# Kernel tuning notes

Measured on AMD Instinct MI355X. Metric: run time of the kernel, lower is better.

The kernel has to match this reference:

```python
import jax, jax.numpy as jnp
from jax import lax
import numpy as np

IMG_H = IMG_W = 1024
STRIDE = 16
FH = FW = 64
C = 512
NA = 9
IOU_T = 0.7
NEG = -1e30
NUM_CLASSES = 21
FV = 4096
POOL = 7


def _make_anchor_map():
    scales = np.array([128.0, 256.0, 512.0])
    ratios = np.array([0.5, 1.0, 2.0])
    ah = (scales[:, None] * np.sqrt(ratios)[None, :]).reshape(-1)  # (9,)
    aw = (scales[:, None] / np.sqrt(ratios)[None, :]).reshape(-1)
    cy = (np.arange(FH) + 0.5) * STRIDE
    cx = (np.arange(FW) + 0.5) * STRIDE
    amap = np.zeros((FH, FW, NA, 4), np.float32)
    amap[..., 0] = cy[:, None, None]
    amap[..., 1] = cx[None, :, None]
    amap[..., 2] = ah
    amap[..., 3] = aw
    return amap.reshape(FH, FW, NA * 4)


def setup_inputs() -> dict:
    key = jax.random.key(0)
    ks = jax.random.split(key, 10)
    flat = POOL * POOL * C
    return {
        "feature_map": jax.random.normal(ks[0], (1, C, FH, FW), jnp.float32),
        "anchor_map": jnp.asarray(_make_anchor_map()),
        "anchor_valid_map": jnp.ones((FH, FW, NA), jnp.float32),
        "rpn_conv1_w": 0.01 * jax.random.normal(ks[1], (C, C, 3, 3), jnp.float32),
        "rpn_conv1_b": jnp.zeros((C,), jnp.float32),
        "rpn_cls_w": 0.01 * jax.random.normal(ks[2], (NA, C, 1, 1), jnp.float32),
        "rpn_cls_b": jnp.zeros((NA,), jnp.float32),
        "rpn_box_w": 0.01 * jax.random.normal(ks[3], (NA * 4, C, 1, 1), jnp.float32),
        "rpn_box_b": jnp.zeros((NA * 4,), jnp.float32),
        "fc1_w": 0.01 * jax.random.normal(ks[4], (FV, flat), jnp.float32),
        "fc1_b": jnp.zeros((FV,), jnp.float32),
        "fc2_w": 0.01 * jax.random.normal(ks[5], (FV, FV), jnp.float32),
        "fc2_b": jnp.zeros((FV,), jnp.float32),
        "cls_w": 0.01 * jax.random.normal(ks[6], (NUM_CLASSES, FV), jnp.float32),
        "cls_b": jnp.zeros((NUM_CLASSES,), jnp.float32),
        "reg_w": 0.001 * jax.random.normal(ks[7], (4 * (NUM_CLASSES - 1), FV), jnp.float32),
        "reg_b": jnp.zeros((4 * (NUM_CLASSES - 1),), jnp.float32),
        "max_proposals_pre_nms": 6000,
        "max_proposals_post_nms": 300,
    }


def _conv(x, w, b):
    y = lax.conv_general_dilated(x, w, (1, 1), 'SAME',
                                 dimension_numbers=('NCHW', 'OIHW', 'NCHW'))
    return y + b[None, :, None, None]


def _roi_pool(fm, rois):
    # fm: (C,H,W); rois: (N,4) as (x1,y1,x2,y2) in pixel coords (torchvision RoIPool semantics)
    Hh, Ww = fm.shape[1], fm.shape[2]
    s = 1.0 / STRIDE
    p = jnp.arange(POOL, dtype=fm.dtype)
    hi = jnp.arange(Hh, dtype=fm.dtype)
    wi = jnp.arange(Ww, dtype=fm.dtype)

    def one(roi):
        x1 = jnp.round(roi[0] * s); y1 = jnp.round(roi[1] * s)
        x2 = jnp.round(roi[2] * s); y2 = jnp.round(roi[3] * s)
        rw = jnp.maximum(x2 - x1 + 1.0, 1.0)
        rh = jnp.maximum(y2 - y1 + 1.0, 1.0)
        bh = rh / POOL; bw = rw / POOL
        hstart = jnp.clip(jnp.floor(p * bh) + y1, 0, Hh)
        hend = jnp.clip(jnp.ceil((p + 1) * bh) + y1, 0, Hh)
        wstart = jnp.clip(jnp.floor(p * bw) + x1, 0, Ww)
        wend = jnp.clip(jnp.ceil((p + 1) * bw) + x1, 0, Ww)
        mh = (hi[None, :] >= hstart[:, None]) & (hi[None, :] < hend[:, None])  # (7,H)
        mw = (wi[None, :] >= wstart[:, None]) & (wi[None, :] < wend[:, None])  # (7,W)
        # max over w per (c,h,pw), then max over h per (c,ph,pw)
        t1 = jnp.max(jnp.where(mw[None, None, :, :], fm[:, :, None, :], NEG), axis=-1)  # (C,H,7)
        t2 = jnp.max(jnp.where(mh[None, :, :, None], t1[:, None, :, :], NEG), axis=2)   # (C,7,7)
        return jnp.where(t2 < NEG / 2, 0.0, t2)  # empty bins -> 0

    return lax.map(one, rois)  # (N,C,7,7)


def reference(feature_map, anchor_map, anchor_valid_map,
              rpn_conv1_w, rpn_conv1_b, rpn_cls_w, rpn_cls_b, rpn_box_w, rpn_box_b,
              fc1_w, fc1_b, fc2_w, fc2_b, cls_w, cls_b, reg_w, reg_b,
              max_proposals_pre_nms, max_proposals_post_nms):
    # ---- RPN heads ----
    y = jax.nn.relu(_conv(feature_map, rpn_conv1_w, rpn_conv1_b))
    scores_map = jax.nn.sigmoid(_conv(y, rpn_cls_w, rpn_cls_b)).transpose(0, 2, 3, 1)   # (1,H,W,9)
    deltas_map = _conv(y, rpn_box_w, rpn_box_b).transpose(0, 2, 3, 1)                   # (1,H,W,36)

    # ---- proposals from anchors + deltas (allow_edge_proposals=True: keep all) ----
    anchors = anchor_map.reshape(-1, 4)        # (cy,cx,h,w)
    scores = scores_map.reshape(-1)
    deltas = deltas_map.reshape(-1, 4)         # (ty,tx,th,tw)
    ctr = anchors[:, 0:2] + deltas[:, 0:2] * anchors[:, 2:4]
    sz = anchors[:, 2:4] * jnp.exp(deltas[:, 2:4])
    boxes = jnp.concatenate([ctr - 0.5 * sz, ctr + 0.5 * sz], axis=1)  # (y1,x1,y2,x2)
    hi_clip = jnp.array([IMG_H - 1, IMG_W - 1, IMG_H - 1, IMG_W - 1], boxes.dtype)
    boxes = jnp.clip(boxes, 0.0, hi_clip)

    # ---- top-k pre-NMS ----
    sc_pre, idx = lax.top_k(scores, max_proposals_pre_nms)
    bx = boxes[idx]

    # ---- NMS (IoU 0.7), score-sorted sequential suppression ----
    area = (bx[:, 2] - bx[:, 0]) * (bx[:, 3] - bx[:, 1])
    yy1 = jnp.maximum(bx[:, None, 0], bx[None, :, 0])
    xx1 = jnp.maximum(bx[:, None, 1], bx[None, :, 1])
    yy2 = jnp.minimum(bx[:, None, 2], bx[None, :, 2])
    xx2 = jnp.minimum(bx[:, None, 3], bx[None, :, 3])
    inter = jnp.clip(yy2 - yy1, 0.0) * jnp.clip(xx2 - xx1, 0.0)
    iou = inter / (area[:, None] + area[None, :] - inter + 1e-8)
    n = max_proposals_pre_nms
    jidx = jnp.arange(n)

    def body(i, sup):
        return sup | ((~sup[i]) & (iou[i] > IOU_T) & (jidx > i))

    sup = lax.fori_loop(0, n, body, jnp.zeros((n,), bool))
    kept_scores = jnp.where(sup, -jnp.inf, sc_pre)
    _, idx2 = lax.top_k(kept_scores, max_proposals_post_nms)
    proposals = lax.stop_gradient(bx[idx2])  # (N,4) (y1,x1,y2,x2); detached as in original

    # ---- detector head: RoIPool + FC stack ----
    rois = proposals[:, jnp.array([1, 0, 3, 2])]       # -> (x1,y1,x2,y2)
    pooled = _roi_pool(feature_map[0], rois)           # (N,C,7,7)
    flat = pooled.reshape(pooled.shape[0], -1)
    h1 = jax.nn.relu(flat @ fc1_w.T + fc1_b)
    h2 = jax.nn.relu(h1 @ fc2_w.T + fc2_b)
    classes = jax.nn.softmax(h2 @ cls_w.T + cls_b, axis=1)          # (N,21)
    box_deltas = h2 @ reg_w.T + reg_b                               # (N,80)
    return (scores_map, deltas_map, proposals, classes, box_deltas)
```

## Files before the change

kernel.cpp:

```cpp
#include <hip/hip_runtime.h>
#include <stdint.h>

typedef float f32x4 __attribute__((ext_vector_type(4)));
typedef short s16x8 __attribute__((ext_vector_type(8)));
typedef unsigned long long u64;

__device__ __forceinline__ unsigned short f2bf(float f) {
  union { float f; unsigned u; } v; v.f = f;
  unsigned u = v.u;
  return (unsigned short)((u + 0x7FFFu + ((u >> 16) & 1u)) >> 16);
}
__device__ __forceinline__ float bf2f(unsigned short b) {
  union { unsigned u; float f; } v; v.u = ((unsigned)b) << 16; return v.f;
}

#define CONV_ICC 8
__global__ __launch_bounds__(256, 2) void k_conv3(const float* __restrict__ fm,
                                                  const float* __restrict__ w,
                                                  float* __restrict__ ypart) {
  __shared__ float Xs[CONV_ICC * 342];
  __shared__ float Ws[CONV_ICC * 9 * 64];
  int bid = blockIdx.x;
  int s = bid & 3, ocg = (bid >> 2) & 7, sp = bid >> 5;
  int h0 = (sp >> 2) * 16, w0 = (sp & 3) * 16;
  int oc0 = ocg * 64;
  int t = threadIdx.x;
  int g = t >> 5, p = t & 31;
  int row = p >> 1, colb = (p & 1) * 8;
  float acc[8][8] = {};
  int cbase = s * 128;
  for (int chunk = 0; chunk < 16; chunk++) {
    int c0 = cbase + chunk * CONV_ICC;
    for (int idx = t; idx < CONV_ICC * 324; idx += 256) {
      int ic = idx / 324, rem = idx - ic * 324;
      int r = rem / 18, cc = rem - r * 18;
      int gy = h0 + r - 1, gx = w0 + cc - 1;
      float v = 0.f;
      if ((unsigned)gy < 64u && (unsigned)gx < 64u) v = fm[(c0 + ic) * 4096 + gy * 64 + gx];
      Xs[ic * 342 + r * 19 + cc] = v;
    }
    for (int idx = t; idx < CONV_ICC * 9 * 64; idx += 256) {
      int oc = idx & 63, rest = idx >> 6;
      int ic = rest / 9, k = rest - ic * 9;
      Ws[idx] = w[(u64)(oc0 + oc) * 4608 + (c0 + ic) * 9 + k];
    }
    __syncthreads();
    for (int ic = 0; ic < CONV_ICC; ic++) {
      const float* xb = &Xs[ic * 342 + colb];
      float xr[3][10];
      #pragma unroll
      for (int r = 0; r < 3; r++)
        #pragma unroll
        for (int j = 0; j < 10; j++)
          xr[r][j] = xb[(row + r) * 19 + j];
      #pragma unroll
      for (int kh = 0; kh < 3; kh++) {
        #pragma unroll
        for (int kw = 0; kw < 3; kw++) {
          const float* wp = &Ws[(ic * 9 + kh * 3 + kw) * 64 + g * 8];
          f32x4 wa = *(const f32x4*)wp;
          f32x4 wb = *(const f32x4*)(wp + 4);
          float wv[8] = {wa.x, wa.y, wa.z, wa.w, wb.x, wb.y, wb.z, wb.w};
          #pragma unroll
          for (int o = 0; o < 8; o++) {
            #pragma unroll
            for (int j = 0; j < 8; j++) {
              acc[o][j] += wv[o] * xr[kh][kw + j];
            }
          }
        }
      }
    }
    __syncthreads();
  }
  float* yp = ypart + (u64)s * 2097152;
  #pragma unroll
  for (int j = 0; j < 8; j++) {
    int pxg = (h0 + row) * 64 + (w0 + colb + j);
    f32x4 v0, v1;
    v0.x = acc[0][j]; v0.y = acc[1][j]; v0.z = acc[2][j]; v0.w = acc[3][j];
    v1.x = acc[4][j]; v1.y = acc[5][j]; v1.z = acc[6][j]; v1.w = acc[7][j];
    f32x4* dst = (f32x4*)&yp[(u64)pxg * 512 + oc0 + g * 8];
    dst[0] = v0; dst[1] = v1;
  }
}

__global__ __launch_bounds__(256) void k_rpn1x1(const float* __restrict__ ypart,
                                                const float* __restrict__ conv_b,
                                                const float* __restrict__ cw, const float* __restrict__ cb,
                                                const float* __restrict__ bw, const float* __restrict__ bb,
                                                float* __restrict__ out_s, float* __restrict__ out_d) {
  __shared__ float Ys[16 * 516];
  int px0 = blockIdx.x * 16;
  int t = threadIdx.x;
  for (int c = t; c < 16 * 128; c += 256) {
    int p = c >> 7, seg = c & 127;
    u64 off = (u64)(px0 + p) * 512 + seg * 4;
    f32x4 v0 = *(const f32x4*)&ypart[off];
    f32x4 v1 = *(const f32x4*)&ypart[2097152 + off];
    f32x4 v2 = *(const f32x4*)&ypart[2 * 2097152 + off];
    f32x4 v3 = *(const f32x4*)&ypart[3 * (u64)2097152 + off];
    f32x4 b = *(const f32x4*)&conv_b[seg * 4];
    f32x4 r;
    r.x = fmaxf(v0.x + v1.x + v2.x + v3.x + b.x, 0.f);
    r.y = fmaxf(v0.y + v1.y + v2.y + v3.y + b.y, 0.f);
    r.z = fmaxf(v0.z + v1.z + v2.z + v3.z + b.z, 0.f);
    r.w = fmaxf(v0.w + v1.w + v2.w + v3.w + b.w, 0.f);
    *(f32x4*)&Ys[p * 516 + seg * 4] = r;
  }
  __syncthreads();
  int px = t & 15, og = t >> 4;
  const float* yr = &Ys[px * 516];
  for (int n = og; n < 45; n += 16) {
    const float* wr = (n < 9) ? &cw[n * 512] : &bw[(n - 9) * 512];
    float acc = 0.f;
    for (int k = 0; k < 512; k += 4) {
      f32x4 wv = *(const f32x4*)&wr[k];
      acc += wv.x * yr[k] + wv.y * yr[k + 1] + wv.z * yr[k + 2] + wv.w * yr[k + 3];
    }
    int gpx = px0 + px;
    if (n < 9) {
      float s = acc + cb[n];
      out_s[gpx * 9 + n] = 1.f / (1.f + expf(-s));
    } else {
      out_d[gpx * 36 + (n - 9)] = acc + bb[n - 9];
    }
  }
}

__global__ void k_decode(const float* __restrict__ sc, const float* __restrict__ dl,
                         const float* __restrict__ amap,
                         float* __restrict__ boxes, u64* __restrict__ keys) {
  int i = blockIdx.x * 256 + threadIdx.x;
  if (i >= 65536) return;
  if (i < 36864) {
    int px = i / 9, a = i - px * 9;
    const float* A = &amap[i * 4];
    const float* D = &dl[px * 36 + a * 4];
    float cy = A[0] + D[0] * A[2];
    float cx = A[1] + D[1] * A[3];
    float hh = A[2] * expf(D[2]);
    float ww = A[3] * expf(D[3]);
    float y1 = fminf(fmaxf(cy - 0.5f * hh, 0.f), 1023.f);
    float x1 = fminf(fmaxf(cx - 0.5f * ww, 0.f), 1023.f);
    float y2 = fminf(fmaxf(cy + 0.5f * hh, 0.f), 1023.f);
    float x2 = fminf(fmaxf(cx + 0.5f * ww, 0.f), 1023.f);
    f32x4 v; v.x = y1; v.y = x1; v.z = y2; v.w = x2;
    *(f32x4*)&boxes[i * 4] = v;
    unsigned bits = __float_as_uint(sc[i]);
    u64 key = ((u64)bits << 16) | (u64)(0xFFFFu - (unsigned)i);
    keys[i] = ~key;
  } else {
    keys[i] = ~0ull;
  }
}

__global__ __launch_bounds__(1024) void k_sort_local(u64* __restrict__ keys) {
  __shared__ u64 S[8192];
  int base = blockIdx.x * 8192;
  for (int i = threadIdx.x; i < 8192; i += 1024) S[i] = keys[base + i];
  __syncthreads();
  for (int k = 2; k <= 8192; k <<= 1) {
    for (int j = k >> 1; j > 0; j >>= 1) {
      for (int p = threadIdx.x; p < 4096; p += 1024) {
        int i = ((p & ~(j - 1)) << 1) | (p & (j - 1));
        int ix = i | j;
        bool up = (((base + i) & k) == 0);
        u64 a = S[i], c = S[ix];
        if ((a > c) == up) { S[i] = c; S[ix] = a; }
      }
      __syncthreads();
    }
  }
  for (int i = threadIdx.x; i < 8192; i += 1024) keys[base + i] = S[i];
}

__global__ void k_sort_global(u64* __restrict__ keys, int k, int j) {
  int p = blockIdx.x * 256 + threadIdx.x;
  int i = ((p & ~(j - 1)) << 1) | (p & (j - 1));
  int ix = i | j;
  bool up = ((i & k) == 0);
  u64 a = keys[i], c = keys[ix];
  if ((a > c) == up) { keys[i] = c; keys[ix] = a; }
}

__global__ __launch_bounds__(1024) void k_sort_merge(u64* __restrict__ keys, int k) {
  __shared__ u64 S[8192];
  int base = blockIdx.x * 8192;
  for (int i = threadIdx.x; i < 8192; i += 1024) S[i] = keys[base + i];
  __syncthreads();
  for (int j = 4096; j > 0; j >>= 1) {
    for (int p = threadIdx.x; p < 4096; p += 1024) {
      int i = ((p & ~(j - 1)) << 1) | (p & (j - 1));
      int ix = i | j;
      bool up = (((base + i) & k) == 0);
      u64 a = S[i], c = S[ix];
      if ((a > c) == up) { S[i] = c; S[ix] = a; }
    }
    __syncthreads();
  }
  for (int i = threadIdx.x; i < 8192; i += 1024) keys[base + i] = S[i];
}

__global__ void k_gather_sorted(const u64* __restrict__ keys, const float* __restrict__ boxes,
                                float* __restrict__ bx) {
  int p = blockIdx.x * 256 + threadIdx.x;
  if (p >= 6000) return;
  u64 key = ~keys[p];
  int idx = 0xFFFF - (int)(key & 0xFFFFull);
  *(f32x4*)&bx[p * 4] = *(const f32x4*)&boxes[idx * 4];
}

__global__ __launch_bounds__(128) void k_nms_mask(const float* __restrict__ bx, u64* __restrict__ mask) {
  int i = blockIdx.x;
  int w = threadIdx.x;
  if (w >= 94) return;
  f32x4 bi = *(const f32x4*)&bx[i * 4];
  float ai = (bi.z - bi.x) * (bi.w - bi.y);
  u64 m = 0;
  int j0 = w * 64;
  for (int b = 0; b < 64; b++) {
    int j = j0 + b;
    if (j >= 6000) break;
    if (j <= i) continue;
    f32x4 bj = *(const f32x4*)&bx[j * 4];
    float yy1 = fmaxf(bi.x, bj.x), xx1 = fmaxf(bi.y, bj.y);
    float yy2 = fminf(bi.z, bj.z), xx2 = fminf(bi.w, bj.w);
    float inter = fmaxf(yy2 - yy1, 0.f) * fmaxf(xx2 - xx1, 0.f);
    float aj = (bj.z - bj.x) * (bj.w - bj.y);
    float iou = inter / (ai + aj - inter + 1e-8f);
    if (iou > 0.7f) m |= (1ull << b);
  }
  mask[i * 94 + w] = m;
}

__global__ __launch_bounds__(64) void k_nms_scan(const u64* __restrict__ mask, int* __restrict__ sel) {
  int lane = threadIdx.x;
  u64 rem0 = 0, rem1 = 0;
  int nkeep = 0;
  u64 cur0[16], cur1[16], nxt0[16], nxt1[16];
  bool l30 = (lane < 30);
  #pragma unroll
  for (int r = 0; r < 16; r++) {
    cur0[r] = mask[r * 94 + lane];
    cur1[r] = l30 ? mask[r * 94 + 64 + lane] : 0ull;
  }
  for (int c0 = 0; c0 < 6000; c0 += 16) {
    int n0 = c0 + 16;
    if (n0 < 6000) {
      #pragma unroll
      for (int r = 0; r < 16; r++) {
        nxt0[r] = mask[(n0 + r) * 94 + lane];
        nxt1[r] = l30 ? mask[(n0 + r) * 94 + 64 + lane] : 0ull;
      }
    }
    #pragma unroll
    for (int r = 0; r < 16; r++) {
      int i = c0 + r;
      int wi = i >> 6, bi = i & 63;
      u64 wv = (wi < 64) ? __shfl(rem0, wi, 64) : __shfl(rem1, wi - 64, 64);
      if (!((wv >> bi) & 1ull)) {
        if (lane == 0 && nkeep < 300) sel[nkeep] = i;
        nkeep++;
        rem0 |= cur0[r]; rem1 |= cur1[r];
      }
    }
    if (nkeep >= 300) return;
    #pragma unroll
    for (int r = 0; r < 16; r++) { cur0[r] = nxt0[r]; cur1[r] = nxt1[r]; }
  }
  __shared__ u64 remS[94];
  remS[lane] = rem0;
  if (l30) remS[64 + lane] = rem1;
  __syncthreads();
  if (lane == 0) {
    int k = nkeep;
    for (int i = 0; i < 6000 && k < 300; i++) {
      if ((remS[i >> 6] >> (i & 63)) & 1ull) sel[k++] = i;
    }
  }
}

__global__ void k_gather_prop(const int* __restrict__ sel, const float* __restrict__ bx,
                              float* __restrict__ out_p, float* __restrict__ rois) {
  int r = blockIdx.x * 64 + threadIdx.x;
  if (r >= 300) return;
  int p = sel[r];
  float y1 = bx[p * 4 + 0], x1 = bx[p * 4 + 1], y2 = bx[p * 4 + 2], x2 = bx[p * 4 + 3];
  out_p[r * 4 + 0] = y1; out_p[r * 4 + 1] = x1; out_p[r * 4 + 2] = y2; out_p[r * 4 + 3] = x2;
  rois[r * 4 + 0] = x1; rois[r * 4 + 1] = y1; rois[r * 4 + 2] = x2; rois[r * 4 + 3] = y2;
}

__global__ __launch_bounds__(256) void k_roipool(const float* __restrict__ fm,
                                                 const float* __restrict__ rois,
                                                 unsigned short* __restrict__ pooled) {
  int roi = blockIdx.x / 98;
  int seg = blockIdx.x - roi * 98;
  __shared__ int hs[7], he[7], wls[7], wle[7];
  if (threadIdx.x < 28) {
    int kind = threadIdx.x / 7, p = threadIdx.x - kind * 7;
    float x1 = rintf(rois[roi * 4 + 0] * 0.0625f);
    float y1 = rintf(rois[roi * 4 + 1] * 0.0625f);
    float x2 = rintf(rois[roi * 4 + 2] * 0.0625f);
    float y2 = rintf(rois[roi * 4 + 3] * 0.0625f);
    float rw = fmaxf(x2 - x1 + 1.f, 1.f), rh = fmaxf(y2 - y1 + 1.f, 1.f);
    float bh = rh / 7.f, bw = rw / 7.f;
    float fp = (float)p;
    if (kind == 0) hs[p]  = (int)fminf(fmaxf(floorf(fp * bh) + y1, 0.f), 64.f);
    if (kind == 1) he[p]  = (int)fminf(fmaxf(ceilf((fp + 1.f) * bh) + y1, 0.f), 64.f);
    if (kind == 2) wls[p] = (int)fminf(fmaxf(floorf(fp * bw) + x1, 0.f), 64.f);
    if (kind == 3) wle[p] = (int)fminf(fmaxf(ceilf((fp + 1.f) * bw) + x1, 0.f), 64.f);
  }
  __syncthreads();
  int o = seg * 256 + threadIdx.x;
  int c = o / 49; int cell = o - c * 49;
  int ph = cell / 7, pw = cell - ph * 7;
  int y0 = hs[ph], y1e = he[ph], x0 = wls[pw], x1e = wle[pw];
  bool any = (y1e > y0) && (x1e > x0);
  float m = -1e30f;
  const float* base = &fm[c * 4096];
  for (int yy = y0; yy < y1e; yy++)
    for (int xx = x0; xx < x1e; xx++)
      m = fmaxf(m, base[yy * 64 + xx]);
  pooled[(u64)roi * 25088 + o] = f2bf(any ? m : 0.f);
}

__global__ __launch_bounds__(512, 2) void k_gemm3(const unsigned short* __restrict__ A,
                                                  const float* __restrict__ B,
                                                  float* __restrict__ Cpre,
                                                  int K, int Kslice, int N) {
  __shared__ uint4 Ab[2][2560];
  __shared__ uint4 Bb[2][1024];
  int n0 = blockIdx.x * 128;
  int s = blockIdx.y;
  int t = threadIdx.x;
  int wave = t >> 6, lane = t & 63;
  int mg = wave & 1, ng = wave >> 1;
  int m0 = mg * 160;
  int lr = lane & 15, lk = lane >> 4;

  int am[5], aks[5];
  #pragma unroll
  for (int i = 0; i < 5; i++) { int idx = t + i * 512; am[i] = idx % 320; aks[i] = idx / 320; }
  int brow = t >> 2, bpart = t & 3;
  const float* gB = &B[(u64)(n0 + brow) * K + bpart * 16];

  f32x4 acc[10][2];
  #pragma unroll
  for (int mt = 0; mt < 10; mt++)
    for (int nt = 0; nt < 2; nt++) { acc[mt][nt].x = 0; acc[mt][nt].y = 0; acc[mt][nt].z = 0; acc[mt][nt].w = 0; }

  int kbeg = s * Kslice;
  int nt_iters = Kslice >> 6;
  uint4 Araw[5];
  f32x4 Braw[4];

  #pragma unroll
  for (int i = 0; i < 5; i++)
    Araw[i] = *(const uint4*)&A[(u64)am[i] * K + kbeg + aks[i] * 8];
  #pragma unroll
  for (int q = 0; q < 4; q++)
    Braw[q] = *(const f32x4*)&gB[kbeg + q * 4];
  #pragma unroll
  for (int i = 0; i < 5; i++) Ab[0][t + i * 512] = Araw[i];
  {
    float fv[16] = {Braw[0].x, Braw[0].y, Braw[0].z, Braw[0].w,
                    Braw[1].x, Braw[1].y, Braw[1].z, Braw[1].w,
                    Braw[2].x, Braw[2].y, Braw[2].z, Braw[2].w,
                    Braw[3].x, Braw[3].y, Braw[3].z, Braw[3].w};
    #pragma unroll
    for (int h = 0; h < 2; h++) {
      s16x8 pk;
      #pragma unroll
      for (int j = 0; j < 8; j++) pk[j] = (short)f2bf(fv[h * 8 + j]);
      *(s16x8*)&Bb[0][(bpart * 2 + h) * 128 + brow] = pk;
    }
  }
  __syncthreads();

  int cur = 0;
  int k0 = kbeg;
  for (int it = 0; it < nt_iters; it++) {
    bool pf = (it + 1 < nt_iters);
    if (pf) {
      int kn = k0 + 64;
      #pragma unroll
      for (int i = 0; i < 5; i++)
        Araw[i] = *(const uint4*)&A[(u64)am[i] * K + kn + aks[i] * 8];
      #pragma unroll
      for (int q = 0; q < 4; q++)
        Braw[q] = *(const f32x4*)&gB[kn + q * 4];
    }
    const unsigned short* ab = (const unsigned short*)Ab[cur];
    const unsigned short* bb = (const unsigned short*)Bb[cur];
    #pragma unroll
    for (int ksub = 0; ksub < 2; ksub++) {
      int ks = ksub * 4 + lk;
      s16x8 bf0 = *(const s16x8*)&bb[(u64)(ks * 128 + ng * 32 + lr) * 8];
      s16x8 bf1 = *(const s16x8*)&bb[(u64)(ks * 128 + ng * 32 + 16 + lr) * 8];
      #pragma unroll
      for (int mt = 0; mt < 10; mt++) {
        s16x8 af = *(const s16x8*)&ab[(u64)(ks * 320 + m0 + mt * 16 + lr) * 8];
        acc[mt][0] = __builtin_amdgcn_mfma_f32_16x16x32_bf16(af, bf0, acc[mt][0], 0, 0, 0);
        acc[mt][1] = __builtin_amdgcn_mfma_f32_16x16x32_bf16(af, bf1, acc[mt][1], 0, 0, 0);
      }
    }
    if (pf) {
      #pragma unroll
      for (int i = 0; i < 5; i++) Ab[cur ^ 1][t + i * 512] = Araw[i];
      float fv[16] = {Braw[0].x, Braw[0].y, Braw[0].z, Braw[0].w,
                      Braw[1].x, Braw[1].y, Braw[1].z, Braw[1].w,
                      Braw[2].x, Braw[2].y, Braw[2].z, Braw[2].w,
                      Braw[3].x, Braw[3].y, Braw[3].z, Braw[3].w};
      #pragma unroll
      for (int h = 0; h < 2; h++) {
        s16x8 pk;
        #pragma unroll
        for (int j = 0; j < 8; j++) pk[j] = (short)f2bf(fv[h * 8 + j]);
        *(s16x8*)&Bb[cur ^ 1][(bpart * 2 + h) * 128 + brow] = pk;
      }
    }
    __syncthreads();
    cur ^= 1;
    k0 += 64;
  }

  #pragma unroll
  for (int mt = 0; mt < 10; mt++)
    for (int nt = 0; nt < 2; nt++)
      for (int r = 0; r < 4; r++) {
        int m = m0 + mt * 16 + lk * 4 + r;
        int n = n0 + ng * 32 + nt * 16 + lr;
        atomicAdd(&Cpre[(u64)m * N + n], acc[mt][nt][r]);
      }
}

__global__ void k_bias_relu_bf(const float* __restrict__ pre, const float* __restrict__ bias,
                               unsigned short* __restrict__ outb) {
  int i = blockIdx.x * 256 + threadIdx.x;
  float v = pre[i] + bias[i & 4095];
  outb[i] = f2bf(fmaxf(v, 0.f));
}

__global__ __launch_bounds__(128) void k_head(const unsigned short* __restrict__ h2,
                                              const float* __restrict__ cw, const float* __restrict__ cb,
                                              const float* __restrict__ rw, const float* __restrict__ rb,
                                              float* __restrict__ out_cls, float* __restrict__ out_reg) {
  __shared__ float Hs[4096];
  __shared__ float logits[101];
  __shared__ float es[21];
  int r = blockIdx.x, t = threadIdx.x;
  for (int c = t; c < 512; c += 128) {
    uint4 raw = *(const uint4*)&h2[(u64)r * 4096 + c * 8];
    unsigned short* sp = (unsigned short*)&raw;
    #pragma unroll
    for (int q = 0; q < 8; q++) Hs[c * 8 + q] = bf2f(sp[q]);
  }
  __syncthreads();
  for (int n = t; n < 101; n += 128) {
    const float* wrow = (n < 21) ? &cw[n * 4096] : &rw[(n - 21) * 4096];
    float acc = 0.f;
    for (int k = 0; k < 4096; k += 4) {
      f32x4 wv = *(const f32x4*)&wrow[k];
      acc += wv.x * Hs[k] + wv.y * Hs[k + 1] + wv.z * Hs[k + 2] + wv.w * Hs[k + 3];
    }
    acc += (n < 21) ? cb[n] : rb[n - 21];
    logits[n] = acc;
  }
  __syncthreads();
  if (t < 21) {
    float mx = logits[0];
    for (int q = 1; q < 21; q++) mx = fmaxf(mx, logits[q]);
    es[t] = expf(logits[t] - mx);
  }
  __syncthreads();
  if (t < 21) {
    float sum = 0.f;
    for (int q = 0; q < 21; q++) sum += es[q];
    out_cls[r * 21 + t] = es[t] / sum;
  }
  if (t >= 21 && t < 101) out_reg[r * 80 + (t - 21)] = logits[t];
}

extern "C" void kernel_launch(void* const* d_in, const int* in_sizes, int n_in,
                              void* d_out, int out_size, void* d_ws, size_t ws_size,
                              hipStream_t stream) {
  (void)in_sizes; (void)n_in; (void)out_size; (void)ws_size;
  const float* fm     = (const float*)d_in[0];
  const float* amap   = (const float*)d_in[1];
  const float* conv_w = (const float*)d_in[3];
  const float* conv_b = (const float*)d_in[4];
  const float* cls_w  = (const float*)d_in[5];
  const float* cls_b  = (const float*)d_in[6];
  const float* box_w  = (const float*)d_in[7];
  const float* box_b  = (const float*)d_in[8];
  const float* fc1_w  = (const float*)d_in[9];
  const float* fc1_b  = (const float*)d_in[10];
  const float* fc2_w  = (const float*)d_in[11];
  const float* fc2_b  = (const float*)d_in[12];
  const float* cw     = (const float*)d_in[13];
  const float* cbias  = (const float*)d_in[14];
  const float* rw     = (const float*)d_in[15];
  const float* rbias  = (const float*)d_in[16];

  float* out_s = (float*)d_out;
  float* out_d = out_s + 36864;
  float* out_p = out_d + 147456;
  float* out_c = out_p + 1200;
  float* out_r = out_c + 6300;

  char* ws = (char*)d_ws;
  float* ypart = (float*)(ws + 0);
  u64*   mask  = (u64*)  (ws + 0);
  unsigned short* pooled = (unsigned short*)(ws + 4718592);
  float* boxes = (float*)(ws + 20971520);
  u64*   keys  = (u64*)  (ws + 21561344);
  float* bx    = (float*)(ws + 22085632);
  int*   sel   = (int*)  (ws + 22181632);
  float* rois  = (float*)(ws + 22182912);
  float* h1pre = (float*)(ws + 22282240);
  unsigned short* h1bf = (unsigned short*)(ws + 27525120);
  float* h2pre = h1pre;
  unsigned short* h2bf = (unsigned short*)(ws + 30146560);

  k_conv3<<<512, 256, 0, stream>>>(fm, conv_w, ypart);
  k_rpn1x1<<<256, 256, 0, stream>>>(ypart, conv_b, cls_w, cls_b, box_w, box_b, out_s, out_d);
  k_decode<<<256, 256, 0, stream>>>(out_s, out_d, amap, boxes, keys);

  k_sort_local<<<8, 1024, 0, stream>>>(keys);
  for (int k = 16384; k <= 65536; k <<= 1) {
    for (int j = k >> 1; j >= 8192; j >>= 1)
      k_sort_global<<<128, 256, 0, stream>>>(keys, k, j);
    k_sort_merge<<<8, 1024, 0, stream>>>(keys, k);
  }

  k_gather_sorted<<<24, 256, 0, stream>>>(keys, boxes, bx);
  k_nms_mask<<<6000, 128, 0, stream>>>(bx, mask);
  k_nms_scan<<<1, 64, 0, stream>>>(mask, sel);
  k_gather_prop<<<5, 64, 0, stream>>>(sel, bx, out_p, rois);

  hipMemsetAsync((char*)pooled + (size_t)300 * 25088 * 2, 0, (size_t)20 * 25088 * 2, stream);
  hipMemsetAsync(h1pre, 0, (size_t)320 * 4096 * 4, stream);

  k_roipool<<<300 * 98, 256, 0, stream>>>(fm, rois, pooled);

  k_gemm3<<<dim3(32, 8), 512, 0, stream>>>(pooled, fc1_w, h1pre, 25088, 3136, 4096);
  k_bias_relu_bf<<<5120, 256, 0, stream>>>(h1pre, fc1_b, h1bf);
  hipMemsetAsync(h2pre, 0, (size_t)320 * 4096 * 4, stream);
  k_gemm3<<<dim3(32, 8), 512, 0, stream>>>(h1bf, fc2_w, h2pre, 4096, 512, 4096);
  k_bias_relu_bf<<<5120, 256, 0, stream>>>(h2pre, fc2_b, h2bf);
  k_head<<<300, 128, 0, stream>>>(h2bf, cw, cbias, rw, rbias, out_c, out_r);
}
```

Measured before the change: 1.004 ms.

## Double-buffer conv3x3 shared tiles with register-staged prefetch of next chunk

The 3x3 RPN conv kernel now keeps two shared-memory buffers for the input and weight tiles. Global loads for the next channel chunk are issued into registers before the current chunk is computed, then written to the alternate buffer, so only one barrier is needed per chunk. Load addresses are precomputed once per thread, which removes the repeated div/mod index math. In exchange, shared memory use doubles and about 29 extra staging registers per thread are held across the compute loop, which may cause spills or lower occupancy under launch_bounds(256,2).

```diff
diff --git a/kernel.cpp b/kernel.cpp
--- a/kernel.cpp
+++ b/kernel.cpp
@@ -15,11 +15,11 @@
 }
 
 #define CONV_ICC 8
-__global__ __launch_bounds__(256, 2) void k_conv3(const float* __restrict__ fm,
+__global__ __launch_bounds__(256, 2) void k_conv4(const float* __restrict__ fm,
                                                   const float* __restrict__ w,
                                                   float* __restrict__ ypart) {
-  __shared__ float Xs[CONV_ICC * 342];
-  __shared__ float Ws[CONV_ICC * 9 * 64];
+  __shared__ float Xs[2][CONV_ICC * 342];
+  __shared__ float Ws[2][CONV_ICC * 9 * 64];
   int bid = blockIdx.x;
   int s = bid & 3, ocg = (bid >> 2) & 7, sp = bid >> 5;
   int h0 = (sp >> 2) * 16, w0 = (sp & 3) * 16;
@@ -27,26 +27,66 @@
   int t = threadIdx.x;
   int g = t >> 5, p = t & 31;
   int row = p >> 1, colb = (p & 1) * 8;
-  float acc[8][8] = {};
-  int cbase = s * 128;
-  for (int chunk = 0; chunk < 16; chunk++) {
-    int c0 = cbase + chunk * CONV_ICC;
-    for (int idx = t; idx < CONV_ICC * 324; idx += 256) {
+
+  int xic[11], xoff[11], xlds[11]; bool xval[11], xact[11];
+  #pragma unroll
+  for (int i = 0; i < 11; i++) {
+    int idx = t + i * 256;
+    xact[i] = (idx < CONV_ICC * 324);
+    if (xact[i]) {
       int ic = idx / 324, rem = idx - ic * 324;
       int r = rem / 18, cc = rem - r * 18;
       int gy = h0 + r - 1, gx = w0 + cc - 1;
-      float v = 0.f;
-      if ((unsigned)gy < 64u && (unsigned)gx < 64u) v = fm[(c0 + ic) * 4096 + gy * 64 + gx];
-      Xs[ic * 342 + r * 19 + cc] = v;
-    }
-    for (int idx = t; idx < CONV_ICC * 9 * 64; idx += 256) {
-      int oc = idx & 63, rest = idx >> 6;
-      int ic = rest / 9, k = rest - ic * 9;
-      Ws[idx] = w[(u64)(oc0 + oc) * 4608 + (c0 + ic) * 9 + k];
-    }
-    __syncthreads();
+      xval[i] = ((unsigned)gy < 64u) && ((unsigned)gx < 64u);
+      xic[i] = ic;
+      xoff[i] = xval[i] ? (gy * 64 + gx) : 0;
+      xlds[i] = ic * 342 + r * 19 + cc;
+    } else { xval[i] = false; xic[i] = 0; xoff[i] = 0; xlds[i] = 0; }
+  }
+  u64 wbase[18];
+  #pragma unroll
+  for (int i = 0; i < 18; i++) {
+    int idx = t + i * 256;
+    int oc = idx & 63, rest = idx >> 6;
+    int ic = rest / 9, kk = rest - ic * 9;
+    wbase[i] = (u64)(oc0 + oc) * 4608 + ic * 9 + kk;
+  }
+
+  float acc[8][8] = {};
+  int cbase = s * 128;
+  float XR[11], WR[18];
+
+  {
+    int c0 = cbase;
+    #pragma unroll
+    for (int i = 0; i < 11; i++)
+      XR[i] = xval[i] ? fm[(u64)(c0 + xic[i]) * 4096 + xoff[i]] : 0.f;
+    #pragma unroll
+    for (int i = 0; i < 18; i++)
+      WR[i] = w[wbase[i] + (u64)c0 * 9];
+    #pragma unroll
+    for (int i = 0; i < 11; i++) if (xact[i]) Xs[0][xlds[i]] = XR[i];
+    #pragma unroll
+    for (int i = 0; i < 18; i++) Ws[0][t + i * 256] = WR[i];
+  }
+  __syncthreads();
+
+  int cur = 0;
+  for (int chunk = 0; chunk < 16; chunk++) {
+    bool pf = (chunk < 15);
+    if (pf) {
+      int cn = cbase + (chunk + 1) * CONV_ICC;
+      #pragma unroll
+      for (int i = 0; i < 11; i++)
+        XR[i] = xval[i] ? fm[(u64)(cn + xic[i]) * 4096 + xoff[i]] : 0.f;
+      #pragma unroll
+      for (int i = 0; i < 18; i++)
+        WR[i] = w[wbase[i] + (u64)cn * 9];
+    }
+    const float* XsC = Xs[cur];
+    const float* WsC = Ws[cur];
     for (int ic = 0; ic < CONV_ICC; ic++) {
-      const float* xb = &Xs[ic * 342 + colb];
+      const float* xb = &XsC[ic * 342 + colb];
       float xr[3][10];
       #pragma unroll
       for (int r = 0; r < 3; r++)
@@ -57,7 +97,7 @@
       for (int kh = 0; kh < 3; kh++) {
         #pragma unroll
         for (int kw = 0; kw < 3; kw++) {
-          const float* wp = &Ws[(ic * 9 + kh * 3 + kw) * 64 + g * 8];
+          const float* wp = &WsC[(ic * 9 + kh * 3 + kw) * 64 + g * 8];
           f32x4 wa = *(const f32x4*)wp;
           f32x4 wb = *(const f32x4*)(wp + 4);
           float wv[8] = {wa.x, wa.y, wa.z, wa.w, wb.x, wb.y, wb.z, wb.w};
@@ -71,8 +111,16 @@
         }
       }
     }
+    if (pf) {
+      #pragma unroll
+      for (int i = 0; i < 11; i++) if (xact[i]) Xs[cur ^ 1][xlds[i]] = XR[i];
+      #pragma unroll
+      for (int i = 0; i < 18; i++) Ws[cur ^ 1][t + i * 256] = WR[i];
+    }
     __syncthreads();
-  }
+    cur ^= 1;
+  }
+
   float* yp = ypart + (u64)s * 2097152;
   #pragma unroll
   for (int j = 0; j < 8; j++) {
@@ -523,7 +571,7 @@
   float* h2pre = h1pre;
   unsigned short* h2bf = (unsigned short*)(ws + 30146560);
 
-  k_conv3<<<512, 256, 0, stream>>>(fm, conv_w, ypart);
+  k_conv4<<<512, 256, 0, stream>>>(fm, conv_w, ypart);
   k_rpn1x1<<<256, 256, 0, stream>>>(ypart, conv_b, cls_w, cls_b, box_w, box_b, out_s, out_d);
   k_decode<<<256, 256, 0, stream>>>(out_s, out_d, amap, boxes, keys);
 
```

After: 961.6 us. 1.04x faster.
